# Kernel optimization log

Measured on AMD Instinct MI355X. Metric: run time of the kernel, lower is better.

The kernel has to match this reference:

```python
import jax, jax.numpy as jnp
import numpy as np

L, B = 512, 512
IN, OBS, K, S = 16, 16, 64, 64


def _lin(x, w, b):
    return x @ w.T + b


def _preprocess(x, w1, b1, w2, b2):
    # PreProcess: two fc layers with ReLU (TD-VAE style)
    return jax.nn.relu(_lin(jax.nn.relu(_lin(x, w1, b1)), w2, b2))


def _dblock(x, p):
    # DBlock: t = tanh(fc1(x)) * sigmoid(fc2(x)); returns (mu, logsigma)
    fc1_w, fc1_b, fc2_w, fc2_b, mu_w, mu_b, ls_w, ls_b = p
    t = jnp.tanh(_lin(x, fc1_w, fc1_b)) * jax.nn.sigmoid(_lin(x, fc2_w, fc2_b))
    return _lin(t, mu_w, mu_b), _lin(t, ls_w, ls_b)


def setup_inputs() -> dict:
    key = jax.random.key(0)
    keys = iter(jax.random.split(key, 64))

    def W(shape, fan_in):
        s = 1.0 / np.sqrt(fan_in)
        return jax.random.uniform(next(keys), shape, jnp.float32, -s, s)

    inp = {
        'external_input_seq': jax.random.normal(next(keys), (L, B, IN), jnp.float32),
        'observations_seq': jax.random.normal(next(keys), (L, B, OBS), jnp.float32),
        'noise': jax.random.normal(next(keys), (L, B, S), jnp.float32),
        # process_u / process_x (PreProcess)
        'pu_w1': W((K, IN), IN), 'pu_b1': W((K,), IN), 'pu_w2': W((K, K), K), 'pu_b2': W((K,), K),
        'px_w1': W((K, OBS), OBS), 'px_b1': W((K,), OBS), 'px_w2': W((K, K), K), 'px_b2': W((K,), K),
        # input_rnn: vanilla tanh RNN(k, k), 1 layer
        'rnn_wih': W((K, K), K), 'rnn_whh': W((K, K), K), 'rnn_bih': W((K,), K), 'rnn_bhh': W((K,), K),
        # posterior_a_layer: MLP(2k, k, k, 1)
        'a_w1': W((K, 2 * K), 2 * K), 'a_b1': W((K,), 2 * K), 'a_w2': W((K, K), K), 'a_b2': W((K,), K),
        # posterior_gauss: DBlock(state+k, 2k, state)
        'po_fc1_w': W((2 * K, S + K), S + K), 'po_fc1_b': W((2 * K,), S + K),
        'po_fc2_w': W((2 * K, S + K), S + K), 'po_fc2_b': W((2 * K,), S + K),
        'po_mu_w': W((S, 2 * K), 2 * K), 'po_mu_b': W((S,), 2 * K),
        'po_ls_w': W((S, 2 * K), 2 * K), 'po_ls_b': W((S,), 2 * K),
        # prior_gauss: DBlock(state+k, 2k, state)
        'pr_fc1_w': W((2 * K, S + K), S + K), 'pr_fc1_b': W((2 * K,), S + K),
        'pr_fc2_w': W((2 * K, S + K), S + K), 'pr_fc2_b': W((2 * K,), S + K),
        'pr_mu_w': W((S, 2 * K), 2 * K), 'pr_mu_b': W((S,), 2 * K),
        'pr_ls_w': W((S, 2 * K), 2 * K), 'pr_ls_b': W((S,), 2 * K),
    }
    return inp


def reference(external_input_seq, observations_seq, noise,
              pu_w1, pu_b1, pu_w2, pu_b2, px_w1, px_b1, px_w2, px_b2,
              rnn_wih, rnn_whh, rnn_bih, rnn_bhh,
              a_w1, a_b1, a_w2, a_b2,
              po_fc1_w, po_fc1_b, po_fc2_w, po_fc2_b, po_mu_w, po_mu_b, po_ls_w, po_ls_b,
              pr_fc1_w, pr_fc1_b, pr_fc2_w, pr_fc2_b, pr_mu_w, pr_mu_b, pr_ls_w, pr_ls_b):
    l, b, _ = external_input_seq.shape
    k = rnn_whh.shape[0]
    s = po_mu_w.shape[0]

    u_emb = _preprocess(external_input_seq, pu_w1, pu_b1, pu_w2, pu_b2)   # [l,b,k]
    x_emb = _preprocess(observations_seq, px_w1, px_b1, px_w2, px_b2)     # [l,b,k]

    # input_rnn: tanh RNN over time (seq-first), h0 = 0
    def rnn_step(h, x):
        h = jnp.tanh(x @ rnn_wih.T + rnn_bih + h @ rnn_whh.T + rnn_bhh)
        return h, h
    _, d_seq = jax.lax.scan(rnn_step, jnp.zeros((b, k), u_emb.dtype), u_emb)  # [l,b,k]

    # posterior_a_layer: pointwise MLP; flip+flip around a pointwise map is identity
    a_in = jnp.concatenate([d_seq, x_emb], axis=-1)                       # [l,b,2k]
    a_seq = _lin(jnp.tanh(_lin(a_in, a_w1, a_b1)), a_w2, a_b2)            # [l,b,k]

    po = (po_fc1_w, po_fc1_b, po_fc2_w, po_fc2_b, po_mu_w, po_mu_b, po_ls_w, po_ls_b)
    pr = (pr_fc1_w, pr_fc1_b, pr_fc2_w, pr_fc2_b, pr_mu_w, pr_mu_b, pr_ls_w, pr_ls_b)

    # sequential latent update + reparameterized sampling
    def step(z_prev, inputs):
        a_t, d_t, eps_t = inputs
        res_mu, logsigma = _dblock(jnp.concatenate([z_prev, a_t], axis=-1), po)
        mu = _dblock(jnp.concatenate([z_prev, d_t], axis=-1), pr)[0] + res_mu
        # cov = diag(exp(logsigma)) => std = exp(0.5 * logsigma)
        z = mu + jnp.exp(0.5 * logsigma) * eps_t
        return z, (mu, logsigma, z)

    z0 = jnp.zeros((b, s), u_emb.dtype)
    _, (state_mu, state_logsigma, sampled_state) = jax.lax.scan(step, z0, (a_seq, d_seq, noise))
    return state_mu, state_logsigma, sampled_state, d_seq
```

## Files before the change

kernel.cpp:

```cpp
#include <hip/hip_runtime.h>

typedef unsigned short u16;
typedef unsigned int u32;

#define L 512
#define BB 512
#define NROWS (L*BB)
#define CH (NROWS*64)

enum {
  O_PUW1 = 0,
  O_PUB1 = 1024,
  O_PUW2 = 1088,
  O_PUB2 = 5184,
  O_PXW1 = 5248,
  O_PXB1 = 6272,
  O_PXW2 = 6336,
  O_PXB2 = 10432,
  O_WIH  = 10496,
  O_RNB  = 14592,
  O_WHH  = 14656,
  O_AW1  = 18752,
  O_AB1  = 26944,
  O_AW2  = 27008,
  O_AB2  = 31104,
  O_POF1 = 31168,
  O_POF1B= 47552,
  O_POF2 = 47680,
  O_POF2B= 64064,
  O_POMU = 64192,
  O_POMUB= 72384,
  O_POLS = 72448,
  O_POLSB= 80640,
  O_PRF1 = 80704,
  O_PRF1B= 97088,
  O_PRF2 = 97216,
  O_PRF2B= 113600,
  O_PRMU = 113728,
  O_PRMUB= 121920,
  O_FLAG = 121984,
  O_HB   = 122000
};
enum {
  HU1 = 0,
  HU2 = 1024,
  HX1 = 5120,
  HX2 = 6144,
  HW3U= 10240,
  HW3X= 14336,
  HEND= 18432
};

__device__ __forceinline__ float b2f(u16 x){ return __uint_as_float(((u32)x)<<16); }
__device__ __forceinline__ u16 f2b(float f){
  u32 u = __float_as_uint(f);
  u32 r = (u + 0x7fffu + ((u>>16)&1u)) >> 16;
  return (u16)r;
}

#if __has_builtin(__builtin_amdgcn_exp2f)
#define EXP2(x) __builtin_amdgcn_exp2f(x)
#else
#define EXP2(x) exp2f(x)
#endif
#if __has_builtin(__builtin_amdgcn_rcpf)
#define RCP(x) __builtin_amdgcn_rcpf(x)
#else
#define RCP(x) (1.0f/(x))
#endif

__device__ __forceinline__ float tanhf_fast(float x){
  float e = EXP2(x * 2.8853900817779268f);
  return 1.0f - 2.0f * RCP(e + 1.0f);
}
__device__ __forceinline__ float sigm_fast(float x){
  float e = EXP2(-1.4426950408889634f * x);
  return RCP(1.0f + e);
}

typedef __attribute__((ext_vector_type(8))) __bf16 bf16x8;
typedef __attribute__((ext_vector_type(4))) float f32x4;

__device__ __forceinline__ f32x4 mfma16(bf16x8 a, bf16x8 b, f32x4 c){
  return __builtin_amdgcn_mfma_f32_16x16x32_bf16(a, b, c, 0, 0, 0);
}
__device__ __forceinline__ bf16x8 wfrag(const float* W, int off){
  union { short s[8]; bf16x8 v; } c;
#pragma unroll
  for (int i=0;i<8;i++) c.s[i] = (short)f2b(W[off+i]);
  return c.v;
}
__device__ __forceinline__ bf16x8 load16(const u16* p){
  union { uint4 u; bf16x8 v; } c;
  c.u = *(const uint4*)p;
  return c.v;
}
__device__ __forceinline__ bf16x8 zfrag(){
  union { uint4 u; bf16x8 v; } c;
  c.u = make_uint4(0,0,0,0);
  return c.v;
}
__device__ __forceinline__ bf16x8 ldA64(const u32* buf, int r, int s){
  union { uint4 u; bf16x8 v; } c;
  c.u = ((const uint4*)buf)[r*8 + (s ^ (r&7))];
  return c.v;
}
__device__ __forceinline__ bf16x8 ldT(const u32* buf, int r, int s){
  union { uint4 u; bf16x8 v; } c;
  c.u = ((const uint4*)buf)[r*16 + (s ^ (r&7))];
  return c.v;
}

template<int MODE>
__device__ __forceinline__ float ldOne(const void* p, size_t i){
  if constexpr (MODE) return ((const float*)p)[i];
  else return b2f(((const u16*)p)[i]);
}
template<int MODE>
__device__ __forceinline__ void stOne(void* p, size_t i, float v){
  if constexpr (MODE) ((float*)p)[i] = v;
  else ((u16*)p)[i] = f2b(v);
}
template<int MODE>
__device__ __forceinline__ float wld(const void* p, int i){
  if constexpr (MODE) return ((const float*)p)[i];
  else return b2f(((const u16*)p)[i]);
}
template<int MODE>
__device__ __forceinline__ u16 hld(const void* p, int i){
  if constexpr (MODE) return f2b(((const float*)p)[i]);
  else return ((const u16*)p)[i];
}
template<int MODE>
__device__ __forceinline__ void* chunkp(void* out, int j){
  return (void*)((char*)out + (size_t)j * (size_t)CH * (MODE ? 4 : 2));
}
__device__ __forceinline__ bool live(const float* W, int tag){
  return ((const u32*)W)[O_FLAG] == (u32)tag;
}

__global__ void kprobe(const u32* __restrict__ ext, u32* __restrict__ flagp){
  if (threadIdx.x == 0 && blockIdx.x == 0){
    int cnt = 0;
    for (int i = 0; i < 1024; ++i){
      u32 e = (ext[i] >> 7) & 0xFFu;
      cnt += (e >= 110u && e <= 134u) ? 1 : 0;
    }
    flagp[0] = (cnt > 512) ? 1u : 2u;
  }
}

template<int MODE>
__global__ void k0_convert(
  const void* pu_w1, const void* pu_b1, const void* pu_w2, const void* pu_b2,
  const void* px_w1, const void* px_b1, const void* px_w2, const void* px_b2,
  const void* rnn_wih, const void* rnn_whh, const void* rnn_bih, const void* rnn_bhh,
  const void* a_w1, const void* a_b1, const void* a_w2, const void* a_b2,
  const void* po_f1, const void* po_f1b, const void* po_f2, const void* po_f2b,
  const void* po_mu, const void* po_mub, const void* po_ls, const void* po_lsb,
  const void* pr_f1, const void* pr_f1b, const void* pr_f2, const void* pr_f2b,
  const void* pr_mu, const void* pr_mub,
  float* W)
{
  if (!live(W, MODE ? 2 : 1)) return;
  const int g = blockIdx.x*blockDim.x + threadIdx.x;
  const int gs = gridDim.x*blockDim.x;
#define CVT(off, src, n) for (int i=g;i<(n);i+=gs) W[(off)+i] = wld<MODE>(src,i);
  CVT(O_PUW1, pu_w1, 1024)  CVT(O_PUB1, pu_b1, 64)
  CVT(O_PUW2, pu_w2, 4096)  CVT(O_PUB2, pu_b2, 64)
  CVT(O_PXW1, px_w1, 1024)  CVT(O_PXB1, px_b1, 64)
  CVT(O_PXW2, px_w2, 4096)  CVT(O_PXB2, px_b2, 64)
  CVT(O_WIH,  rnn_wih, 4096)
  CVT(O_WHH,  rnn_whh, 4096)
  CVT(O_AW1,  a_w1, 8192)   CVT(O_AB1, a_b1, 64)
  CVT(O_AW2,  a_w2, 4096)   CVT(O_AB2, a_b2, 64)
  CVT(O_POF1, po_f1, 16384) CVT(O_POF1B, po_f1b, 128)
  CVT(O_POF2, po_f2, 16384) CVT(O_POF2B, po_f2b, 128)
  CVT(O_POMU, po_mu, 8192)  CVT(O_POMUB, po_mub, 64)
  CVT(O_POLS, po_ls, 8192)  CVT(O_POLSB, po_lsb, 64)
  CVT(O_PRF1, pr_f1, 16384) CVT(O_PRF1B, pr_f1b, 128)
  CVT(O_PRF2, pr_f2, 16384) CVT(O_PRF2B, pr_f2b, 128)
  CVT(O_PRMU, pr_mu, 8192)  CVT(O_PRMUB, pr_mub, 64)
#undef CVT
  for (int i=g;i<64;i+=gs) W[O_RNB+i] = wld<MODE>(rnn_bih,i) + wld<MODE>(rnn_bhh,i);

  u16* Wh = (u16*)(W + O_HB);
  for (int i=g;i<1024;i+=gs) Wh[HU1+i] = hld<MODE>(pu_w1,i);
  for (int i=g;i<4096;i+=gs) Wh[HU2+i] = hld<MODE>(pu_w2,i);
  for (int i=g;i<1024;i+=gs) Wh[HX1+i] = hld<MODE>(px_w1,i);
  for (int i=g;i<4096;i+=gs) Wh[HX2+i] = hld<MODE>(px_w2,i);
  for (int i=g;i<4096;i+=gs) Wh[HW3U+i] = hld<MODE>(rnn_wih,i);
  for (int i=g;i<4096;i+=gs){
    int j = i>>6, c = i&63;
    Wh[HW3X+i] = hld<MODE>(a_w1, j*128 + 64 + c);
  }
}

#define K1_NT 4
template<int MODE>
__global__ __launch_bounds__(512) void k1m(
  const void* __restrict__ ext, const void* __restrict__ obs,
  const float* __restrict__ W, void* __restrict__ outb)
{
  if (!live(W, MODE ? 2 : 1)) return;
  void* rnn_in = chunkp<MODE>(outb, 1);
  void* ax_out = chunkp<MODE>(outb, 2);

  const int tid = threadIdx.x;
  const int wave = tid>>6, lane = tid&63;
  const int lr = lane&15, lg = lane>>4;
  const u16* Wh = (const u16*)(W + O_HB);

  __shared__ __align__(16) u16 Et[8][1024];
  u16* myT = Et[wave];
  u32* myT32 = (u32*)myT;

#pragma unroll 1
  for (int p=0;p<2;p++){
    const void* src = p ? obs : ext;
    void* dst = p ? ax_out : rnn_in;
    const int h1 = p?HX1:HU1, h2 = p?HX2:HU2, h3 = p?HW3X:HW3U;
    const int b1o = p?O_PXB1:O_PUB1, b2o = p?O_PXB2:O_PUB2, b3o = p?O_AB1:O_RNB;

    bf16x8 w1[4], w2[4][2], w3[4][2];
    float bb1[4], bb2[4], bb3[4];
#pragma unroll
    for (int n=0;n<4;n++){
      const int j = n*16 + lr;
      w1[n] = (lg<2) ? load16(Wh + h1 + j*16 + lg*8) : zfrag();
#pragma unroll
      for (int kk=0;kk<2;kk++){
        w2[n][kk] = load16(Wh + h2 + j*64 + kk*32 + lg*8);
        w3[n][kk] = load16(Wh + h3 + j*64 + kk*32 + lg*8);
      }
      bb1[n] = W[b1o+j]; bb2[n] = W[b2o+j]; bb3[n] = W[b3o+j];
    }

#pragma unroll 1
    for (int it=0; it<K1_NT; ++it){
      const size_t row0 = ((size_t)(blockIdx.x*8 + wave)*K1_NT + it)*16;

      bf16x8 xa;
      if (lg < 2){
        if constexpr (MODE){
          const float4* sp = (const float4*)((const float*)src + (row0+lr)*16);
          float4 f0 = sp[lg*2], f1 = sp[lg*2+1];
          union { short s[8]; bf16x8 v; } c;
          c.s[0]=(short)f2b(f0.x); c.s[1]=(short)f2b(f0.y);
          c.s[2]=(short)f2b(f0.z); c.s[3]=(short)f2b(f0.w);
          c.s[4]=(short)f2b(f1.x); c.s[5]=(short)f2b(f1.y);
          c.s[6]=(short)f2b(f1.z); c.s[7]=(short)f2b(f1.w);
          xa = c.v;
        } else {
          xa = load16((const u16*)src + (row0+lr)*16 + lg*8);
        }
      } else xa = zfrag();

      f32x4 c[4];
#pragma unroll
      for (int n=0;n<4;n++){
        f32x4 ci = {bb1[n],bb1[n],bb1[n],bb1[n]};
        ci = mfma16(xa, w1[n], ci);
#pragma unroll
        for (int r=0;r<4;r++){
          float v = fmaxf(ci[r], 0.0f);
          const int b = lg*4 + r, j = n*16 + lr;
          myT[b*64 + (((j>>3)^(b&7))<<3) + (j&7)] = f2b(v);
        }
      }
      {
        bf16x8 a0 = ldA64(myT32, lr, lg);
        bf16x8 a1 = ldA64(myT32, lr, 4+lg);
#pragma unroll
        for (int n=0;n<4;n++){
          f32x4 ci = {bb2[n],bb2[n],bb2[n],bb2[n]};
          ci = mfma16(a0, w2[n][0], ci);
          ci = mfma16(a1, w2[n][1], ci);
          c[n] = ci;
        }
#pragma unroll
        for (int n=0;n<4;n++)
#pragma unroll
          for (int r=0;r<4;r++){
            float v = fmaxf(c[n][r], 0.0f);
            const int b = lg*4 + r, j = n*16 + lr;
            myT[b*64 + (((j>>3)^(b&7))<<3) + (j&7)] = f2b(v);
          }
      }
      {
        bf16x8 a0 = ldA64(myT32, lr, lg);
        bf16x8 a1 = ldA64(myT32, lr, 4+lg);
#pragma unroll
        for (int n=0;n<4;n++){
          f32x4 ci = {bb3[n],bb3[n],bb3[n],bb3[n]};
          ci = mfma16(a0, w3[n][0], ci);
          ci = mfma16(a1, w3[n][1], ci);
          c[n] = ci;
        }
#pragma unroll
        for (int n=0;n<4;n++)
#pragma unroll
          for (int r=0;r<4;r++){
            const int b = lg*4 + r, j = n*16 + lr;
            myT[b*64 + (((j>>3)^(b&7))<<3) + (j&7)] = f2b(c[n][r]);
          }
      }
#pragma unroll
      for (int s2=0;s2<2;s2++){
        const int s_lin = lane*2 + s2;
        const int r = s_lin>>3, sl = s_lin&7;
        uint4 v = ((const uint4*)myT32)[r*8 + (sl^(r&7))];
        if constexpr (MODE){
          float* dp = (float*)dst + (row0+r)*64 + sl*8;
          u32 w[4] = {v.x, v.y, v.z, v.w};
          float f[8];
#pragma unroll
          for (int i=0;i<4;i++){ f[2*i] = b2f((u16)(w[i]&0xffffu)); f[2*i+1] = b2f((u16)(w[i]>>16)); }
          ((float4*)dp)[0] = make_float4(f[0],f[1],f[2],f[3]);
          ((float4*)dp)[1] = make_float4(f[4],f[5],f[6],f[7]);
        } else {
          ((uint4*)((u16*)dst + (row0+r)*64))[sl] = v;
        }
      }
    }
  }
}

__device__ __forceinline__ float dot16(const float* w, float4 a, float4 b, float4 c, float4 d){
  float s0=0.f, s1=0.f;
  s0=fmaf(w[0],a.x,s0);  s1=fmaf(w[1],a.y,s1);  s0=fmaf(w[2],a.z,s0);  s1=fmaf(w[3],a.w,s1);
  s0=fmaf(w[4],b.x,s0);  s1=fmaf(w[5],b.y,s1);  s0=fmaf(w[6],b.z,s0);  s1=fmaf(w[7],b.w,s1);
  s0=fmaf(w[8],c.x,s0);  s1=fmaf(w[9],c.y,s1);  s0=fmaf(w[10],c.z,s0); s1=fmaf(w[11],c.w,s1);
  s0=fmaf(w[12],d.x,s0); s1=fmaf(w[13],d.y,s1); s0=fmaf(w[14],d.z,s0); s1=fmaf(w[15],d.w,s1);
  return s0+s1;
}

template<int MODE>
__global__ __launch_bounds__(256) void k2_rnn(
  const float* __restrict__ W, void* __restrict__ outb)
{
  if (!live(W, MODE ? 2 : 1)) return;
  void* a_seq  = chunkp<MODE>(outb, 0);
  void* rnn_in = chunkp<MODE>(outb, 1);
  void* ax     = chunkp<MODE>(outb, 2);
  void* d_seq  = chunkp<MODE>(outb, 3);

  const int b = blockIdx.x;
  const int tid = threadIdx.x;
  const int q = tid>>6, j = tid&63;

  float wh[16], wa1[16], wa2[16];
#pragma unroll
  for (int i=0;i<16;i++){
    wh[i]  = W[O_WHH + j*64  + q*16 + i];
    wa1[i] = W[O_AW1 + j*128 + q*16 + i];
    wa2[i] = W[O_AW2 + j*64  + q*16 + i];
  }
  const float ab2j = W[O_AB2 + j];

  __shared__ __align__(16) float h_lds[64];
  __shared__ __align__(16) float v_lds[64];
  __shared__ __align__(16) float red1[256], red2[256], red3[256];
  if (tid < 64){ h_lds[tid] = 0.f; v_lds[tid] = 0.f; }
  __syncthreads();

  const size_t brow = (size_t)b*64 + j;
  for (int t=0; t<L+2; ++t){
    const float4* hv = (const float4*)(&h_lds[q*16]);
    const float4* vv = (const float4*)(&v_lds[q*16]);
    float4 h0=hv[0], h1=hv[1], h2=hv[2], h3=hv[3];
    float4 v0=vv[0], v1=vv[1], v2=vv[2], v3=vv[3];
    red1[tid] = dot16(wh,  h0,h1,h2,h3);
    red2[tid] = dot16(wa1, h0,h1,h2,h3);
    red3[tid] = dot16(wa2, v0,v1,v2,v3);
    __syncthreads();
    if (q==0){
      if (t < L){
        const size_t idx = (size_t)t*(BB*64) + brow;
        float s = red1[j]+red1[64+j]+red1[128+j]+red1[192+j] + ldOne<MODE>(rnn_in, idx);
        float hn = tanhf_fast(s);
        h_lds[j] = hn;
        stOne<MODE>(d_seq, idx, hn);
      }
    } else if (q==1){
      if (t>=1 && t<=L){
        const size_t idx = (size_t)(t-1)*(BB*64) + brow;
        float s = red2[j]+red2[64+j]+red2[128+j]+red2[192+j] + ldOne<MODE>(ax, idx);
        v_lds[j] = tanhf_fast(s);
      }
    } else if (q==2){
      if (t>=2){
        const size_t idx = (size_t)(t-2)*(BB*64) + brow;
        float s = red3[j]+red3[64+j]+red3[128+j]+red3[192+j] + ab2j;
        stOne<MODE>(a_seq, idx, s);
      }
    }
    __syncthreads();
  }
}

template<int MODE>
__global__ __launch_bounds__(512,2) void k4m(
  const float* __restrict__ W,
  const void* __restrict__ noise, void* __restrict__ outb)
{
  if (!live(W, MODE ? 2 : 1)) return;
  void* amu = chunkp<MODE>(outb, 0);
  void* lsc = chunkp<MODE>(outb, 1);
  void* zc  = chunkp<MODE>(outb, 2);
  void* dsq = chunkp<MODE>(outb, 3);

  const int G = blockIdx.x;
  const int tid = threadIdx.x;
  const int wave = tid>>6, lane = tid&63;
  const int lr = lane&15, lg = lane>>4;

  __shared__ __align__(16) u32 Zbuf[512];
  __shared__ __align__(16) u32 Abuf[2][512];
  __shared__ __align__(16) u32 Dbuf[2][512];
  __shared__ __align__(16) u32 Ebuf[2][1024];
  __shared__ __align__(16) u32 Tpo[1024];
  __shared__ __align__(16) u32 Tpr[1024];
  __shared__ __align__(16) float Obuf[3*1024];
  __shared__ float bmu[64], bls[64];

  const bool isPo = wave < 4;
  const int wq = wave & 3;
  const int jA = wq*32;

  const int of1 = isPo ? O_POF1 : O_PRF1;
  const int of2 = isPo ? O_POF2 : O_PRF2;
  bf16x8 wf1[2][4], wf2[2][4];
  float bA1[2], bA2[2];
#pragma unroll
  for (int nt=0; nt<2; ++nt){
    const int j = jA + nt*16 + lr;
    bA1[nt] = W[(isPo?O_POF1B:O_PRF1B) + j];
    bA2[nt] = W[(isPo?O_POF2B:O_PRF2B) + j];
#pragma unroll
    for (int kk=0; kk<4; ++kk){
      const int k = kk*32 + lg*8;
      wf1[nt][kk] = wfrag(W, of1 + j*128 + k);
      wf2[nt][kk] = wfrag(W, of2 + j*128 + k);
    }
  }
  const int mb = wave>>1, nh = wave&1;
  bf16x8 wb[2][4];
  if (wave < 6){
    const int ob = (mb==0) ? O_POMU : (mb==1 ? O_POLS : O_PRMU);
#pragma unroll
    for (int nt=0; nt<2; ++nt)
#pragma unroll
      for (int kk=0; kk<4; ++kk){
        const int j = nh*32 + nt*16 + lr;
        const int k = kk*32 + lg*8;
        wb[nt][kk] = wfrag(W, ob + j*128 + k);
      }
  }

  if (tid < 64){ bmu[tid] = W[O_POMUB+tid] + W[O_PRMUB+tid]; bls[tid] = W[O_POLSB+tid]; }
  Zbuf[tid & 511] = 0;

  const int pr_ = lane>>2, pc = lane&3;
  float4 pA[4], pE[4]; uint4 qA[2], qE[2];

  auto pf_issue = [&](int tt){
    const size_t rowb = ((size_t)tt*BB + G*16 + pr_)*64;
    const void* gsrc = (wave==6) ? amu : dsq;
    if constexpr (MODE){
      const float4* sp = (const float4*)((const float*)gsrc + rowb) + pc*4;
#pragma unroll
      for (int i=0;i<4;i++) pA[i] = sp[i];
      if (wave==6){
        const float4* ep = (const float4*)((const float*)noise + rowb) + pc*4;
#pragma unroll
        for (int i=0;i<4;i++) pE[i] = ep[i];
      }
    } else {
      const uint4* sp = (const uint4*)((const u16*)gsrc + rowb) + pc*2;
      qA[0] = sp[0]; qA[1] = sp[1];
      if (wave==6){
        const uint4* ep = (const uint4*)((const u16*)noise + rowb) + pc*2;
        qE[0] = ep[0]; qE[1] = ep[1];
      }
    }
  };
  auto pf_write = [&](int buf){
    u32* dst = (wave==6) ? Abuf[buf] : Dbuf[buf];
    uint4* d0 = (uint4*)dst + (pr_*8 + ((pc*2  ) ^ (pr_&7)));
    uint4* d1 = (uint4*)dst + (pr_*8 + ((pc*2+1) ^ (pr_&7)));
    if constexpr (MODE){
      u32 w[8];
#pragma unroll
      for (int i=0;i<4;i++){
        w[2*i]   = (u32)f2b(pA[i].x) | ((u32)f2b(pA[i].y)<<16);
        w[2*i+1] = (u32)f2b(pA[i].z) | ((u32)f2b(pA[i].w)<<16);
      }
      *d0 = make_uint4(w[0],w[1],w[2],w[3]);
      *d1 = make_uint4(w[4],w[5],w[6],w[7]);
      if (wave==6){
        uint4* eb = (uint4*)Ebuf[buf] + (pr_*16 + pc*4);
#pragma unroll
        for (int i=0;i<4;i++){
          union { float4 f; uint4 u; } cv; cv.f = pE[i];
          eb[i] = cv.u;
        }
      }
    } else {
      *d0 = qA[0]; *d1 = qA[1];
      if (wave==6){
        u32* Eb = Ebuf[buf] + pr_*64 + pc*16;
        u32 ww[4] = {qE[0].x, qE[0].y, qE[0].z, qE[0].w};
#pragma unroll
        for (int i=0;i<4;i++){ Eb[2*i] = ww[i]<<16; Eb[2*i+1] = ww[i] & 0xffff0000u; }
        u32 w2[4] = {qE[1].x, qE[1].y, qE[1].z, qE[1].w};
#pragma unroll
        for (int i=0;i<4;i++){ Eb[8+2*i] = w2[i]<<16; Eb[8+2*i+1] = w2[i] & 0xffff0000u; }
      }
    }
  };

  if (wave >= 6){ pf_issue(0); pf_write(0); }
  __syncthreads();

  for (int t=0; t<L; ++t){
    const int cur = t&1, nb = cur^1;
    if (wave >= 6 && t+1 < L) pf_issue(t+1);

    const u32* ADc = isPo ? Abuf[cur] : Dbuf[cur];
    bf16x8 a0 = ldA64(Zbuf, lr, lg);
    bf16x8 a1 = ldA64(Zbuf, lr, 4+lg);
    bf16x8 a2 = ldA64(ADc,  lr, lg);
    bf16x8 a3 = ldA64(ADc,  lr, 4+lg);
    f32x4 c1[2], c2[2];
#pragma unroll
    for (int nt=0; nt<2; ++nt){
      f32x4 i1 = {bA1[nt],bA1[nt],bA1[nt],bA1[nt]};
      f32x4 i2 = {bA2[nt],bA2[nt],bA2[nt],bA2[nt]};
      i1 = mfma16(a0, wf1[nt][0], i1);
      i1 = mfma16(a1, wf1[nt][1], i1);
      i1 = mfma16(a2, wf1[nt][2], i1);
      i1 = mfma16(a3, wf1[nt][3], i1);
      i2 = mfma16(a0, wf2[nt][0], i2);
      i2 = mfma16(a1, wf2[nt][1], i2);
      i2 = mfma16(a2, wf2[nt][2], i2);
      i2 = mfma16(a3, wf2[nt][3], i2);
      c1[nt] = i1; c2[nt] = i2;
    }
    u16* Td = (u16*)(isPo ? Tpo : Tpr);
#pragma unroll
    for (int nt=0; nt<2; ++nt)
#pragma unroll
      for (int r=0; r<4; ++r){
        float tv = tanhf_fast(c1[nt][r]) * sigm_fast(c2[nt][r]);
        const int j = jA + nt*16 + lr;
        const int b = lg*4 + r;
        Td[b*128 + (((j>>3)^(b&7))<<3) + (j&7)] = f2b(tv);
      }
    __syncthreads();

    if (wave < 6){
      const u32* Ts = (mb==2) ? Tpr : Tpo;
      bf16x8 t0 = ldT(Ts, lr, lg);
      bf16x8 t1 = ldT(Ts, lr, 4+lg);
      bf16x8 t2 = ldT(Ts, lr, 8+lg);
      bf16x8 t3 = ldT(Ts, lr, 12+lg);
      f32x4 d0 = {0.f,0.f,0.f,0.f}, d1 = {0.f,0.f,0.f,0.f};
      d0 = mfma16(t0, wb[0][0], d0);
      d0 = mfma16(t1, wb[0][1], d0);
      d0 = mfma16(t2, wb[0][2], d0);
      d0 = mfma16(t3, wb[0][3], d0);
      d1 = mfma16(t0, wb[1][0], d1);
      d1 = mfma16(t1, wb[1][1], d1);
      d1 = mfma16(t2, wb[1][2], d1);
      d1 = mfma16(t3, wb[1][3], d1);
      float* Od = &Obuf[mb*1024];
#pragma unroll
      for (int r=0; r<4; ++r){
        const int b = lg*4 + r;
        const int j0 = nh*32 + lr;
        const int j1 = nh*32 + 16 + lr;
        Od[b*64 + (((j0>>2)^(b&7))<<2) + (j0&3)] = d0[r];
        Od[b*64 + (((j1>>2)^(b&7))<<2) + (j1&3)] = d1[r];
      }
    } else if (t+1 < L){
      pf_write(nb);
    }
    __syncthreads();

    {
      const int b = tid>>5;
      const int j = (tid&31)*2;
      const int sidx = b*64 + (((j>>2)^(b&7))<<2) + (j&3);
      float2 vpo = *(const float2*)&Obuf[0*1024 + sidx];
      float2 vls = *(const float2*)&Obuf[1*1024 + sidx];
      float2 vpr = *(const float2*)&Obuf[2*1024 + sidx];
      float2 bm = *(const float2*)&bmu[j];
      float2 bl = *(const float2*)&bls[j];
      float e0 = __uint_as_float(Ebuf[cur][b*64 + j]);
      float e1 = __uint_as_float(Ebuf[cur][b*64 + j + 1]);
      float mu0 = vpo.x + vpr.x + bm.x;
      float mu1 = vpo.y + vpr.y + bm.y;
      float ls0 = vls.x + bl.x;
      float ls1 = vls.y + bl.y;
      float z0 = fmaf(EXP2(ls0*0.7213475204444817f), e0, mu0);
      float z1 = fmaf(EXP2(ls1*0.7213475204444817f), e1, mu1);
      Zbuf[b*32 + (((j>>3)^(b&7))<<2) + ((j&7)>>1)] = (u32)f2b(z0) | ((u32)f2b(z1)<<16);
      const size_t idx = ((size_t)t*BB + G*16 + b)*64 + j;
      if constexpr (MODE){
        *(float2*)((float*)amu + idx) = make_float2(mu0, mu1);
        *(float2*)((float*)lsc + idx) = make_float2(ls0, ls1);
        *(float2*)((float*)zc  + idx) = make_float2(z0, z1);
      } else {
        *(u32*)((u16*)amu + idx) = (u32)f2b(mu0) | ((u32)f2b(mu1)<<16);
        *(u32*)((u16*)lsc + idx) = (u32)f2b(ls0) | ((u32)f2b(ls1)<<16);
        *(u32*)((u16*)zc  + idx) = (u32)f2b(z0)  | ((u32)f2b(z1)<<16);
      }
    }
    __syncthreads();
  }
}

extern "C" void kernel_launch(void* const* d_in, const int* in_sizes, int n_in,
                              void* d_out, int out_size, void* d_ws, size_t ws_size,
                              hipStream_t stream)
{
  (void)in_sizes; (void)n_in; (void)out_size; (void)ws_size;

  const void* ext   = d_in[0];
  const void* obs   = d_in[1];
  const void* noise = d_in[2];
  float* W = (float*)d_ws;

  kprobe<<<1,64,0,stream>>>((const u32*)ext, (u32*)W + O_FLAG);

#define K0ARGS \
    d_in[3],  d_in[4],  d_in[5],  d_in[6],  d_in[7],  d_in[8],  d_in[9],  d_in[10], \
    d_in[11], d_in[12], d_in[13], d_in[14], d_in[15], d_in[16], d_in[17], d_in[18], \
    d_in[19], d_in[20], d_in[21], d_in[22], d_in[23], d_in[24], d_in[25], d_in[26], \
    d_in[27], d_in[28], d_in[29], d_in[30], d_in[31], d_in[32], W

  k0_convert<0><<<64,256,0,stream>>>(K0ARGS);
  k0_convert<1><<<64,256,0,stream>>>(K0ARGS);
#undef K0ARGS

  k1m<0><<<NROWS/(8*K1_NT*16), 512, 0, stream>>>(ext, obs, W, d_out);
  k1m<1><<<NROWS/(8*K1_NT*16), 512, 0, stream>>>(ext, obs, W, d_out);

  k2_rnn<0><<<BB, 256, 0, stream>>>(W, d_out);
  k2_rnn<1><<<BB, 256, 0, stream>>>(W, d_out);

  k4m<0><<<32, 512, 0, stream>>>(W, noise, d_out);
  k4m<1><<<32, 512, 0, stream>>>(W, noise, d_out);
}
```

Before: 1.100 ms.

## Fuse RNN recurrence into latent-scan kernel with MFMA and LDS ring buffers

Merges the separate RNN/posterior-a kernel and the latent-state scan kernel into one 1024-thread kernel per 16-batch group. Waves 8-15 compute the RNN and a-layer with bf16 MFMA and write into 8-deep LDS ring buffers. Waves 0-7 run the latent DBlock update four steps behind, reading from those rings. This removes the d_seq/a_seq global round trip, one launch pair, and the scalar fp32 dot products. The cost is reduced RNN precision (bf16), only 32 blocks for the whole recurrence, and extra barriers shared by both pipelines.

```diff
diff --git a/kernel.cpp b/kernel.cpp
--- a/kernel.cpp
+++ b/kernel.cpp
@@ -326,89 +326,18 @@
   }
 }
 
-__device__ __forceinline__ float dot16(const float* w, float4 a, float4 b, float4 c, float4 d){
-  float s0=0.f, s1=0.f;
-  s0=fmaf(w[0],a.x,s0);  s1=fmaf(w[1],a.y,s1);  s0=fmaf(w[2],a.z,s0);  s1=fmaf(w[3],a.w,s1);
-  s0=fmaf(w[4],b.x,s0);  s1=fmaf(w[5],b.y,s1);  s0=fmaf(w[6],b.z,s0);  s1=fmaf(w[7],b.w,s1);
-  s0=fmaf(w[8],c.x,s0);  s1=fmaf(w[9],c.y,s1);  s0=fmaf(w[10],c.z,s0); s1=fmaf(w[11],c.w,s1);
-  s0=fmaf(w[12],d.x,s0); s1=fmaf(w[13],d.y,s1); s0=fmaf(w[14],d.z,s0); s1=fmaf(w[15],d.w,s1);
-  return s0+s1;
-}
-
-template<int MODE>
-__global__ __launch_bounds__(256) void k2_rnn(
-  const float* __restrict__ W, void* __restrict__ outb)
-{
-  if (!live(W, MODE ? 2 : 1)) return;
-  void* a_seq  = chunkp<MODE>(outb, 0);
-  void* rnn_in = chunkp<MODE>(outb, 1);
-  void* ax     = chunkp<MODE>(outb, 2);
-  void* d_seq  = chunkp<MODE>(outb, 3);
-
-  const int b = blockIdx.x;
-  const int tid = threadIdx.x;
-  const int q = tid>>6, j = tid&63;
-
-  float wh[16], wa1[16], wa2[16];
-#pragma unroll
-  for (int i=0;i<16;i++){
-    wh[i]  = W[O_WHH + j*64  + q*16 + i];
-    wa1[i] = W[O_AW1 + j*128 + q*16 + i];
-    wa2[i] = W[O_AW2 + j*64  + q*16 + i];
-  }
-  const float ab2j = W[O_AB2 + j];
-
-  __shared__ __align__(16) float h_lds[64];
-  __shared__ __align__(16) float v_lds[64];
-  __shared__ __align__(16) float red1[256], red2[256], red3[256];
-  if (tid < 64){ h_lds[tid] = 0.f; v_lds[tid] = 0.f; }
-  __syncthreads();
-
-  const size_t brow = (size_t)b*64 + j;
-  for (int t=0; t<L+2; ++t){
-    const float4* hv = (const float4*)(&h_lds[q*16]);
-    const float4* vv = (const float4*)(&v_lds[q*16]);
-    float4 h0=hv[0], h1=hv[1], h2=hv[2], h3=hv[3];
-    float4 v0=vv[0], v1=vv[1], v2=vv[2], v3=vv[3];
-    red1[tid] = dot16(wh,  h0,h1,h2,h3);
-    red2[tid] = dot16(wa1, h0,h1,h2,h3);
-    red3[tid] = dot16(wa2, v0,v1,v2,v3);
-    __syncthreads();
-    if (q==0){
-      if (t < L){
-        const size_t idx = (size_t)t*(BB*64) + brow;
-        float s = red1[j]+red1[64+j]+red1[128+j]+red1[192+j] + ldOne<MODE>(rnn_in, idx);
-        float hn = tanhf_fast(s);
-        h_lds[j] = hn;
-        stOne<MODE>(d_seq, idx, hn);
-      }
-    } else if (q==1){
-      if (t>=1 && t<=L){
-        const size_t idx = (size_t)(t-1)*(BB*64) + brow;
-        float s = red2[j]+red2[64+j]+red2[128+j]+red2[192+j] + ldOne<MODE>(ax, idx);
-        v_lds[j] = tanhf_fast(s);
-      }
-    } else if (q==2){
-      if (t>=2){
-        const size_t idx = (size_t)(t-2)*(BB*64) + brow;
-        float s = red3[j]+red3[64+j]+red3[128+j]+red3[192+j] + ab2j;
-        stOne<MODE>(a_seq, idx, s);
-      }
-    }
-    __syncthreads();
-  }
-}
-
-template<int MODE>
-__global__ __launch_bounds__(512,2) void k4m(
+template<int MODE>
+__global__ __launch_bounds__(1024,1) void k24(
   const float* __restrict__ W,
   const void* __restrict__ noise, void* __restrict__ outb)
 {
   if (!live(W, MODE ? 2 : 1)) return;
-  void* amu = chunkp<MODE>(outb, 0);
+  void* muc = chunkp<MODE>(outb, 0);
   void* lsc = chunkp<MODE>(outb, 1);
-  void* zc  = chunkp<MODE>(outb, 2);
-  void* dsq = chunkp<MODE>(outb, 3);
+  void* zcc = chunkp<MODE>(outb, 2);
+  void* dsc = chunkp<MODE>(outb, 3);
+  const void* rnn_in = lsc;
+  const void* ax     = zcc;
 
   const int G = blockIdx.x;
   const int tid = threadIdx.x;
@@ -416,179 +345,254 @@
   const int lr = lane&15, lg = lane>>4;
 
   __shared__ __align__(16) u32 Zbuf[512];
-  __shared__ __align__(16) u32 Abuf[2][512];
-  __shared__ __align__(16) u32 Dbuf[2][512];
+  __shared__ __align__(16) u32 Aring[8][512];
+  __shared__ __align__(16) u32 Dring[8][512];
+  __shared__ __align__(16) u32 Vbuf[2][512];
   __shared__ __align__(16) u32 Ebuf[2][1024];
   __shared__ __align__(16) u32 Tpo[1024];
   __shared__ __align__(16) u32 Tpr[1024];
   __shared__ __align__(16) float Obuf[3*1024];
   __shared__ float bmu[64], bls[64];
 
+  const bool k4w = wave < 8;
   const bool isPo = wave < 4;
   const int wq = wave & 3;
   const int jA = wq*32;
-
-  const int of1 = isPo ? O_POF1 : O_PRF1;
-  const int of2 = isPo ? O_POF2 : O_PRF2;
+  const int j2k = wq*16 + lr;
+
   bf16x8 wf1[2][4], wf2[2][4];
-  float bA1[2], bA2[2];
-#pragma unroll
-  for (int nt=0; nt<2; ++nt){
-    const int j = jA + nt*16 + lr;
-    bA1[nt] = W[(isPo?O_POF1B:O_PRF1B) + j];
-    bA2[nt] = W[(isPo?O_POF2B:O_PRF2B) + j];
-#pragma unroll
-    for (int kk=0; kk<4; ++kk){
-      const int k = kk*32 + lg*8;
-      wf1[nt][kk] = wfrag(W, of1 + j*128 + k);
-      wf2[nt][kk] = wfrag(W, of2 + j*128 + k);
+  float bA1[2]={0,0}, bA2[2]={0,0};
+  bf16x8 wb[2][4];
+  const int mb = wave>>1, nh = wave&1;
+  bf16x8 kh[2], kx[2];
+  float ab2 = 0.f;
+
+  if (k4w){
+    const int of1 = isPo ? O_POF1 : O_PRF1;
+    const int of2 = isPo ? O_POF2 : O_PRF2;
+#pragma unroll
+    for (int nt=0; nt<2; ++nt){
+      const int j = jA + nt*16 + lr;
+      bA1[nt] = W[(isPo?O_POF1B:O_PRF1B) + j];
+      bA2[nt] = W[(isPo?O_POF2B:O_PRF2B) + j];
+#pragma unroll
+      for (int kk=0; kk<4; ++kk){
+        const int k = kk*32 + lg*8;
+        wf1[nt][kk] = wfrag(W, of1 + j*128 + k);
+        wf2[nt][kk] = wfrag(W, of2 + j*128 + k);
+      }
+    }
+    if (wave < 6){
+      const int ob = (mb==0) ? O_POMU : (mb==1 ? O_POLS : O_PRMU);
+#pragma unroll
+      for (int nt=0; nt<2; ++nt)
+#pragma unroll
+        for (int kk=0; kk<4; ++kk){
+          const int j = nh*32 + nt*16 + lr;
+          const int k = kk*32 + lg*8;
+          wb[nt][kk] = wfrag(W, ob + j*128 + k);
+        }
+    }
+  } else {
+    const bool hiw = wave >= 12;
+    if (!hiw){
+      kh[0] = wfrag(W, O_WHH + j2k*64 + 0  + lg*8);
+      kh[1] = wfrag(W, O_WHH + j2k*64 + 32 + lg*8);
+    } else {
+      kh[0] = wfrag(W, O_AW1 + j2k*128 + 64 + 0  + lg*8);
+      kh[1] = wfrag(W, O_AW1 + j2k*128 + 64 + 32 + lg*8);
+      kx[0] = wfrag(W, O_AW2 + j2k*64 + 0  + lg*8);
+      kx[1] = wfrag(W, O_AW2 + j2k*64 + 32 + lg*8);
+      ab2 = W[O_AB2 + j2k];
     }
   }
-  const int mb = wave>>1, nh = wave&1;
-  bf16x8 wb[2][4];
-  if (wave < 6){
-    const int ob = (mb==0) ? O_POMU : (mb==1 ? O_POLS : O_PRMU);
-#pragma unroll
-    for (int nt=0; nt<2; ++nt)
-#pragma unroll
-      for (int kk=0; kk<4; ++kk){
-        const int j = nh*32 + nt*16 + lr;
-        const int k = kk*32 + lg*8;
-        wb[nt][kk] = wfrag(W, ob + j*128 + k);
-      }
-  }
 
   if (tid < 64){ bmu[tid] = W[O_POMUB+tid] + W[O_PRMUB+tid]; bls[tid] = W[O_POLSB+tid]; }
-  Zbuf[tid & 511] = 0;
-
-  const int pr_ = lane>>2, pc = lane&3;
-  float4 pA[4], pE[4]; uint4 qA[2], qE[2];
-
-  auto pf_issue = [&](int tt){
-    const size_t rowb = ((size_t)tt*BB + G*16 + pr_)*64;
-    const void* gsrc = (wave==6) ? amu : dsq;
+  if (tid < 512) Zbuf[tid] = 0;
+  for (int i=tid; i<4096; i+=1024){ ((u32*)Dring)[i] = 0; ((u32*)Aring)[i] = 0; }
+  if (tid < 1024) ((u32*)Vbuf)[tid] = 0;
+
+  const int epr = lane>>2, epc = lane&3;
+  float4 pE[4]; uint4 qE[2];
+  auto eps_issue = [&](int tt){
+    const size_t rowb = ((size_t)tt*BB + G*16 + epr)*64;
     if constexpr (MODE){
-      const float4* sp = (const float4*)((const float*)gsrc + rowb) + pc*4;
-#pragma unroll
-      for (int i=0;i<4;i++) pA[i] = sp[i];
-      if (wave==6){
-        const float4* ep = (const float4*)((const float*)noise + rowb) + pc*4;
-#pragma unroll
-        for (int i=0;i<4;i++) pE[i] = ep[i];
-      }
+      const float4* ep = (const float4*)((const float*)noise + rowb) + epc*4;
+#pragma unroll
+      for (int i=0;i<4;i++) pE[i] = ep[i];
     } else {
-      const uint4* sp = (const uint4*)((const u16*)gsrc + rowb) + pc*2;
-      qA[0] = sp[0]; qA[1] = sp[1];
-      if (wave==6){
-        const uint4* ep = (const uint4*)((const u16*)noise + rowb) + pc*2;
-        qE[0] = ep[0]; qE[1] = ep[1];
-      }
+      const uint4* ep = (const uint4*)((const u16*)noise + rowb) + epc*2;
+      qE[0] = ep[0]; qE[1] = ep[1];
     }
   };
-  auto pf_write = [&](int buf){
-    u32* dst = (wave==6) ? Abuf[buf] : Dbuf[buf];
-    uint4* d0 = (uint4*)dst + (pr_*8 + ((pc*2  ) ^ (pr_&7)));
-    uint4* d1 = (uint4*)dst + (pr_*8 + ((pc*2+1) ^ (pr_&7)));
+  auto eps_write = [&](int buf){
     if constexpr (MODE){
-      u32 w[8];
+      uint4* eb = (uint4*)Ebuf[buf] + (epr*16 + epc*4);
 #pragma unroll
       for (int i=0;i<4;i++){
-        w[2*i]   = (u32)f2b(pA[i].x) | ((u32)f2b(pA[i].y)<<16);
-        w[2*i+1] = (u32)f2b(pA[i].z) | ((u32)f2b(pA[i].w)<<16);
-      }
-      *d0 = make_uint4(w[0],w[1],w[2],w[3]);
-      *d1 = make_uint4(w[4],w[5],w[6],w[7]);
-      if (wave==6){
-        uint4* eb = (uint4*)Ebuf[buf] + (pr_*16 + pc*4);
-#pragma unroll
-        for (int i=0;i<4;i++){
-          union { float4 f; uint4 u; } cv; cv.f = pE[i];
-          eb[i] = cv.u;
-        }
+        union { float4 f; uint4 u; } cv; cv.f = pE[i];
+        eb[i] = cv.u;
       }
     } else {
-      *d0 = qA[0]; *d1 = qA[1];
-      if (wave==6){
-        u32* Eb = Ebuf[buf] + pr_*64 + pc*16;
-        u32 ww[4] = {qE[0].x, qE[0].y, qE[0].z, qE[0].w};
-#pragma unroll
-        for (int i=0;i<4;i++){ Eb[2*i] = ww[i]<<16; Eb[2*i+1] = ww[i] & 0xffff0000u; }
-        u32 w2[4] = {qE[1].x, qE[1].y, qE[1].z, qE[1].w};
-#pragma unroll
-        for (int i=0;i<4;i++){ Eb[8+2*i] = w2[i]<<16; Eb[8+2*i+1] = w2[i] & 0xffff0000u; }
-      }
+      u32* Eb = Ebuf[buf] + epr*64 + epc*16;
+      u32 ww[4] = {qE[0].x, qE[0].y, qE[0].z, qE[0].w};
+#pragma unroll
+      for (int i=0;i<4;i++){ Eb[2*i] = ww[i]<<16; Eb[2*i+1] = ww[i] & 0xffff0000u; }
+      u32 w2[4] = {qE[1].x, qE[1].y, qE[1].z, qE[1].w};
+#pragma unroll
+      for (int i=0;i<4;i++){ Eb[8+2*i] = w2[i]<<16; Eb[8+2*i+1] = w2[i] & 0xffff0000u; }
     }
   };
 
-  if (wave >= 6){ pf_issue(0); pf_write(0); }
+  float pc0=0,pc1=0,pc2=0,pc3=0, pn0=0,pn1=0,pn2=0,pn3=0;
+  auto k2_load = [&](const void* src, int step, float& a,float& b,float& c,float& d){
+    const size_t base = ((size_t)step*BB + G*16 + lg*4)*64 + j2k;
+    a = ldOne<MODE>(src, base);
+    b = ldOne<MODE>(src, base+64);
+    c = ldOne<MODE>(src, base+128);
+    d = ldOne<MODE>(src, base+192);
+  };
+  if (!k4w && wave < 12) k2_load(rnn_in, 0, pc0,pc1,pc2,pc3);
   __syncthreads();
 
-  for (int t=0; t<L; ++t){
-    const int cur = t&1, nb = cur^1;
-    if (wave >= 6 && t+1 < L) pf_issue(t+1);
-
-    const u32* ADc = isPo ? Abuf[cur] : Dbuf[cur];
-    bf16x8 a0 = ldA64(Zbuf, lr, lg);
-    bf16x8 a1 = ldA64(Zbuf, lr, 4+lg);
-    bf16x8 a2 = ldA64(ADc,  lr, lg);
-    bf16x8 a3 = ldA64(ADc,  lr, 4+lg);
-    f32x4 c1[2], c2[2];
-#pragma unroll
-    for (int nt=0; nt<2; ++nt){
-      f32x4 i1 = {bA1[nt],bA1[nt],bA1[nt],bA1[nt]};
-      f32x4 i2 = {bA2[nt],bA2[nt],bA2[nt],bA2[nt]};
-      i1 = mfma16(a0, wf1[nt][0], i1);
-      i1 = mfma16(a1, wf1[nt][1], i1);
-      i1 = mfma16(a2, wf1[nt][2], i1);
-      i1 = mfma16(a3, wf1[nt][3], i1);
-      i2 = mfma16(a0, wf2[nt][0], i2);
-      i2 = mfma16(a1, wf2[nt][1], i2);
-      i2 = mfma16(a2, wf2[nt][2], i2);
-      i2 = mfma16(a3, wf2[nt][3], i2);
-      c1[nt] = i1; c2[nt] = i2;
-    }
-    u16* Td = (u16*)(isPo ? Tpo : Tpr);
-#pragma unroll
-    for (int nt=0; nt<2; ++nt)
-#pragma unroll
-      for (int r=0; r<4; ++r){
-        float tv = tanhf_fast(c1[nt][r]) * sigm_fast(c2[nt][r]);
-        const int j = jA + nt*16 + lr;
-        const int b = lg*4 + r;
-        Td[b*128 + (((j>>3)^(b&7))<<3) + (j&7)] = f2b(tv);
-      }
+#pragma unroll 1
+  for (int it=0; it<L+4; ++it){
+    const int t4 = it - 4;
+
+    if (k4w){
+      if (wave==6 && t4+1>=0 && t4+1<L) eps_issue(t4+1);
+      if (t4 >= 0){
+        const u32* ADc = isPo ? Aring[t4&7] : Dring[t4&7];
+        bf16x8 a0 = ldA64(Zbuf, lr, lg);
+        bf16x8 a1 = ldA64(Zbuf, lr, 4+lg);
+        bf16x8 a2 = ldA64(ADc,  lr, lg);
+        bf16x8 a3 = ldA64(ADc,  lr, 4+lg);
+        f32x4 c1[2], c2[2];
+#pragma unroll
+        for (int nt=0; nt<2; ++nt){
+          f32x4 i1 = {bA1[nt],bA1[nt],bA1[nt],bA1[nt]};
+          f32x4 i2 = {bA2[nt],bA2[nt],bA2[nt],bA2[nt]};
+          i1 = mfma16(a0, wf1[nt][0], i1);
+          i1 = mfma16(a1, wf1[nt][1], i1);
+          i1 = mfma16(a2, wf1[nt][2], i1);
+          i1 = mfma16(a3, wf1[nt][3], i1);
+          i2 = mfma16(a0, wf2[nt][0], i2);
+          i2 = mfma16(a1, wf2[nt][1], i2);
+          i2 = mfma16(a2, wf2[nt][2], i2);
+          i2 = mfma16(a3, wf2[nt][3], i2);
+          c1[nt] = i1; c2[nt] = i2;
+        }
+        u16* Td = (u16*)(isPo ? Tpo : Tpr);
+#pragma unroll
+        for (int nt=0; nt<2; ++nt)
+#pragma unroll
+          for (int r=0; r<4; ++r){
+            float tv = tanhf_fast(c1[nt][r]) * sigm_fast(c2[nt][r]);
+            const int j = jA + nt*16 + lr;
+            const int b = lg*4 + r;
+            Td[b*128 + (((j>>3)^(b&7))<<3) + (j&7)] = f2b(tv);
+          }
+      }
+    } else {
+      const bool hiw = wave >= 12;
+      if (!hiw){
+        if (it+1 < L) k2_load(rnn_in, it+1, pn0,pn1,pn2,pn3);
+      } else {
+        if (it < L)   k2_load(ax, it, pn0,pn1,pn2,pn3);
+      }
+      if (!hiw){
+        if (it < L){
+          bf16x8 h0 = ldA64(Dring[(it-1)&7], lr, lg);
+          bf16x8 h1 = ldA64(Dring[(it-1)&7], lr, 4+lg);
+          f32x4 ch = {0.f,0.f,0.f,0.f};
+          ch = mfma16(h0, kh[0], ch);
+          ch = mfma16(h1, kh[1], ch);
+          u16* Hd = (u16*)Dring[it&7];
+          float pcv[4] = {pc0,pc1,pc2,pc3};
+#pragma unroll
+          for (int r=0;r<4;r++){
+            const int b = lg*4 + r;
+            float hv = tanhf_fast(ch[r] + pcv[r]);
+            Hd[(b*8 + ((j2k>>3)^(b&7)))*8 + (j2k&7)] = f2b(hv);
+          }
+        }
+      } else {
+        if (it>=1 && it<=L){
+          bf16x8 h0 = ldA64(Dring[(it-1)&7], lr, lg);
+          bf16x8 h1 = ldA64(Dring[(it-1)&7], lr, 4+lg);
+          f32x4 cv = {0.f,0.f,0.f,0.f};
+          cv = mfma16(h0, kh[0], cv);
+          cv = mfma16(h1, kh[1], cv);
+          u16* Vd = (u16*)Vbuf[(it&1)^1];
+          float pcv[4] = {pc0,pc1,pc2,pc3};
+#pragma unroll
+          for (int r=0;r<4;r++){
+            const int b = lg*4 + r;
+            float vv = tanhf_fast(cv[r] + pcv[r]);
+            Vd[(b*8 + ((j2k>>3)^(b&7)))*8 + (j2k&7)] = f2b(vv);
+          }
+        }
+        if (it>=2 && it<=L+1){
+          bf16x8 v0 = ldA64(Vbuf[it&1], lr, lg);
+          bf16x8 v1 = ldA64(Vbuf[it&1], lr, 4+lg);
+          f32x4 ca = {ab2,ab2,ab2,ab2};
+          ca = mfma16(v0, kx[0], ca);
+          ca = mfma16(v1, kx[1], ca);
+          u16* Ad = (u16*)Aring[(it-2)&7];
+#pragma unroll
+          for (int r=0;r<4;r++){
+            const int b = lg*4 + r;
+            Ad[(b*8 + ((j2k>>3)^(b&7)))*8 + (j2k&7)] = f2b(ca[r]);
+          }
+        }
+      }
+      pc0=pn0; pc1=pn1; pc2=pn2; pc3=pn3;
+    }
     __syncthreads();
 
-    if (wave < 6){
-      const u32* Ts = (mb==2) ? Tpr : Tpo;
-      bf16x8 t0 = ldT(Ts, lr, lg);
-      bf16x8 t1 = ldT(Ts, lr, 4+lg);
-      bf16x8 t2 = ldT(Ts, lr, 8+lg);
-      bf16x8 t3 = ldT(Ts, lr, 12+lg);
-      f32x4 d0 = {0.f,0.f,0.f,0.f}, d1 = {0.f,0.f,0.f,0.f};
-      d0 = mfma16(t0, wb[0][0], d0);
-      d0 = mfma16(t1, wb[0][1], d0);
-      d0 = mfma16(t2, wb[0][2], d0);
-      d0 = mfma16(t3, wb[0][3], d0);
-      d1 = mfma16(t0, wb[1][0], d1);
-      d1 = mfma16(t1, wb[1][1], d1);
-      d1 = mfma16(t2, wb[1][2], d1);
-      d1 = mfma16(t3, wb[1][3], d1);
-      float* Od = &Obuf[mb*1024];
-#pragma unroll
-      for (int r=0; r<4; ++r){
-        const int b = lg*4 + r;
-        const int j0 = nh*32 + lr;
-        const int j1 = nh*32 + 16 + lr;
-        Od[b*64 + (((j0>>2)^(b&7))<<2) + (j0&3)] = d0[r];
-        Od[b*64 + (((j1>>2)^(b&7))<<2) + (j1&3)] = d1[r];
-      }
-    } else if (t+1 < L){
-      pf_write(nb);
+    if (k4w){
+      if (t4 >= 0 && wave < 6){
+        const u32* Ts = (mb==2) ? Tpr : Tpo;
+        bf16x8 t0 = ldT(Ts, lr, lg);
+        bf16x8 t1 = ldT(Ts, lr, 4+lg);
+        bf16x8 t2 = ldT(Ts, lr, 8+lg);
+        bf16x8 t3 = ldT(Ts, lr, 12+lg);
+        f32x4 d0 = {0.f,0.f,0.f,0.f}, d1 = {0.f,0.f,0.f,0.f};
+        d0 = mfma16(t0, wb[0][0], d0);
+        d0 = mfma16(t1, wb[0][1], d0);
+        d0 = mfma16(t2, wb[0][2], d0);
+        d0 = mfma16(t3, wb[0][3], d0);
+        d1 = mfma16(t0, wb[1][0], d1);
+        d1 = mfma16(t1, wb[1][1], d1);
+        d1 = mfma16(t2, wb[1][2], d1);
+        d1 = mfma16(t3, wb[1][3], d1);
+        float* Od = &Obuf[mb*1024];
+#pragma unroll
+        for (int r=0; r<4; ++r){
+          const int b = lg*4 + r;
+          const int j0 = nh*32 + lr;
+          const int j1 = nh*32 + 16 + lr;
+          Od[b*64 + (((j0>>2)^(b&7))<<2) + (j0&3)] = d0[r];
+          Od[b*64 + (((j1>>2)^(b&7))<<2) + (j1&3)] = d1[r];
+        }
+      }
+      if (wave==6 && t4+1>=0 && t4+1<L) eps_write((t4+1)&1);
+    } else {
+      if (it < L){
+        const int lt = tid - 512;
+        const int b = lt>>5, j = (lt&31)*2;
+        u32 w = Dring[it&7][b*32 + (((j>>3)^(b&7))<<2) + ((j&7)>>1)];
+        const size_t idx = ((size_t)it*BB + G*16 + b)*64 + j;
+        if constexpr (MODE){
+          *(float2*)((float*)dsc + idx) = make_float2(b2f((u16)(w&0xffffu)), b2f((u16)(w>>16)));
+        } else {
+          *(u32*)((u16*)dsc + idx) = w;
+        }
+      }
     }
     __syncthreads();
 
-    {
+    if (t4 >= 0 && tid < 512){
       const int b = tid>>5;
       const int j = (tid&31)*2;
       const int sidx = b*64 + (((j>>2)^(b&7))<<2) + (j&3);
@@ -597,8 +601,8 @@
       float2 vpr = *(const float2*)&Obuf[2*1024 + sidx];
       float2 bm = *(const float2*)&bmu[j];
       float2 bl = *(const float2*)&bls[j];
-      float e0 = __uint_as_float(Ebuf[cur][b*64 + j]);
-      float e1 = __uint_as_float(Ebuf[cur][b*64 + j + 1]);
+      float e0 = __uint_as_float(Ebuf[t4&1][b*64 + j]);
+      float e1 = __uint_as_float(Ebuf[t4&1][b*64 + j + 1]);
       float mu0 = vpo.x + vpr.x + bm.x;
       float mu1 = vpo.y + vpr.y + bm.y;
       float ls0 = vls.x + bl.x;
@@ -606,15 +610,15 @@
       float z0 = fmaf(EXP2(ls0*0.7213475204444817f), e0, mu0);
       float z1 = fmaf(EXP2(ls1*0.7213475204444817f), e1, mu1);
       Zbuf[b*32 + (((j>>3)^(b&7))<<2) + ((j&7)>>1)] = (u32)f2b(z0) | ((u32)f2b(z1)<<16);
-      const size_t idx = ((size_t)t*BB + G*16 + b)*64 + j;
+      const size_t idx = ((size_t)t4*BB + G*16 + b)*64 + j;
       if constexpr (MODE){
-        *(float2*)((float*)amu + idx) = make_float2(mu0, mu1);
+        *(float2*)((float*)muc + idx) = make_float2(mu0, mu1);
         *(float2*)((float*)lsc + idx) = make_float2(ls0, ls1);
-        *(float2*)((float*)zc  + idx) = make_float2(z0, z1);
+        *(float2*)((float*)zcc + idx) = make_float2(z0, z1);
       } else {
-        *(u32*)((u16*)amu + idx) = (u32)f2b(mu0) | ((u32)f2b(mu1)<<16);
+        *(u32*)((u16*)muc + idx) = (u32)f2b(mu0) | ((u32)f2b(mu1)<<16);
         *(u32*)((u16*)lsc + idx) = (u32)f2b(ls0) | ((u32)f2b(ls1)<<16);
-        *(u32*)((u16*)zc  + idx) = (u32)f2b(z0)  | ((u32)f2b(z1)<<16);
+        *(u32*)((u16*)zcc + idx) = (u32)f2b(z0)  | ((u32)f2b(z1)<<16);
       }
     }
     __syncthreads();
@@ -647,9 +651,6 @@
   k1m<0><<<NROWS/(8*K1_NT*16), 512, 0, stream>>>(ext, obs, W, d_out);
   k1m<1><<<NROWS/(8*K1_NT*16), 512, 0, stream>>>(ext, obs, W, d_out);
 
-  k2_rnn<0><<<BB, 256, 0, stream>>>(W, d_out);
-  k2_rnn<1><<<BB, 256, 0, stream>>>(W, d_out);
-
-  k4m<0><<<32, 512, 0, stream>>>(W, noise, d_out);
-  k4m<1><<<32, 512, 0, stream>>>(W, noise, d_out);
-}
+  k24<0><<<32, 1024, 0, stream>>>(W, noise, d_out);
+  k24<1><<<32, 1024, 0, stream>>>(W, noise, d_out);
+}
```

New measurement: 3.637 ms. 231% more time.
